# Kernel tuning notes

Measured on AMD Instinct MI355X. Metric: run time of the kernel, lower is better.

The kernel has to match this reference:

```python
import jax, jax.numpy as jnp
from jax import lax
import numpy as np

B, DIM, H, W = 1, 48, 192, 192
HEADS, K, DIL = 2, 7, 3
HD = DIM // HEADS
HID = int(DIM * 2.66)  # 127 (Restormer GEGLU hidden)
EPS = 1e-5


def _window_starts(L, Kk, D):
    # NATTEN window-start rule: keep phase i % D, shift window inside bounds.
    s = np.zeros(L, dtype=np.int32)
    for i in range(L):
        if D <= 1:
            st = max(i - Kk // 2, 0)
            if i + Kk // 2 >= L:
                st = L - Kk
        else:
            st = i - (Kk // 2) * D
            if st < 0:
                st = i % D
            elif i + (Kk // 2) * D >= L:
                imodd = i % D
                a = (L // D) * D
                b = L - a
                if imodd < b:
                    st = L - b + imodd - 2 * (Kk // 2) * D
                else:
                    st = a + imodd - Kk * D
        s[i] = st
    return s


def _nbr_tables(L, Kk, D):
    st = _window_starts(L, Kk, D)
    idx = st[:, None] + np.arange(Kk)[None, :] * D          # [L, K] absolute neighbor idx
    pb = (st - np.arange(L)) // D                            # signed offset of window start (in dilation units)
    pb = pb[:, None] + (Kk - 1) + np.arange(Kk)[None, :]     # [L, K] rpb index in [0, 2K-2]
    return jnp.asarray(idx), jnp.asarray(pb)

IH, PBH = _nbr_tables(H, K, DIL)
IW, PBW = _nbr_tables(W, K, DIL)


def layernorm(x, w, b):  # channel LN on NCHW (WithBias, biased var)
    mu = x.mean(1, keepdims=True)
    var = ((x - mu) ** 2).mean(1, keepdims=True)
    return (x - mu) / jnp.sqrt(var + EPS) * w[None, :, None, None] + b[None, :, None, None]


def na2d(x, qkv_w, qkv_b, rpb, proj_w, proj_b):
    # x: NCHW -> BHWC
    t = x.transpose(0, 2, 3, 1)
    qkv = t @ qkv_w.T + qkv_b                                # [B,H,W,3*DIM]
    qkv = qkv.reshape(B, H, W, 3, HEADS, HD)
    q, k, v = qkv[:, :, :, 0], qkv[:, :, :, 1], qkv[:, :, :, 2]
    q = q * (HD ** -0.5)
    # gather dilated 7x7 neighborhoods: [B, H, K, W, K, heads, hd]
    kn = k[:, IH[:, :, None, None], IW[None, None, :, :]]
    vn = v[:, IH[:, :, None, None], IW[None, None, :, :]]
    attn = jnp.einsum('bijnc,bixjync->bijnxy', q, kn)        # [B,H,W,heads,K,K]
    bias = rpb[:, PBH][:, :, :, PBW]                         # [heads,H,K,W,K]
    attn = attn + bias.transpose(1, 3, 0, 2, 4)
    attn = jax.nn.softmax(attn.reshape(B, H, W, HEADS, K * K), axis=-1)
    attn = attn.reshape(B, H, W, HEADS, K, K)
    out = jnp.einsum('bijnxy,bixjync->bijnc', attn, vn).reshape(B, H, W, DIM)
    out = out @ proj_w.T + proj_b
    return out.transpose(0, 3, 1, 2)


def chan_mod(x, eca_w):  # ECA-style gate: GAP -> 1D conv over channels -> sigmoid
    p = x.mean((2, 3))                                       # [B,C]
    y = lax.conv_general_dilated(p[:, None, :], eca_w[None, None, :], (1,), [(3, 3)],
                                 dimension_numbers=('NCH', 'OIH', 'NCH'))[:, 0, :]
    return jax.nn.sigmoid(y)[:, :, None, None]


def ffn(x, w_in, w_dw, w_out):  # conv-GEGLU
    t = jnp.einsum('bchw,oc->bohw', x, w_in)                 # 1x1: DIM -> 2*HID
    t = lax.conv_general_dilated(t, w_dw, (1, 1), [(1, 1), (1, 1)],
                                 feature_group_count=2 * HID,
                                 dimension_numbers=('NCHW', 'OIHW', 'NCHW'))
    x1, x2 = t[:, :HID], t[:, HID:]
    g = jax.nn.gelu(x1, approximate=False) * x2
    return jnp.einsum('bchw,oc->bohw', g, w_out)             # 1x1: HID -> DIM


def setup_inputs() -> dict:
    key = jax.random.key(0)
    ks = jax.random.split(key, 10)
    d = {
        'x': jax.random.normal(ks[0], (B, DIM, H, W), jnp.float32),
        'ln1_w': jnp.ones((DIM,), jnp.float32),
        'ln1_b': jnp.zeros((DIM,), jnp.float32),
        'qkv_w': jax.random.normal(ks[1], (3 * DIM, DIM), jnp.float32) * 0.05,
        'qkv_b': jnp.zeros((3 * DIM,), jnp.float32),
        'rpb': jax.random.normal(ks[2], (HEADS, 2 * K - 1, 2 * K - 1), jnp.float32) * 0.02,
        'proj_w': jax.random.normal(ks[3], (DIM, DIM), jnp.float32) * 0.05,
        'proj_b': jnp.zeros((DIM,), jnp.float32),
        'eca_w': jax.random.normal(ks[4], (7,), jnp.float32) * 0.1,
        'ln2_w': jnp.ones((DIM,), jnp.float32),
        'ln2_b': jnp.zeros((DIM,), jnp.float32),
        'w_in': jax.random.normal(ks[5], (2 * HID, DIM), jnp.float32) * 0.05,
        'w_dw': jax.random.normal(ks[6], (2 * HID, 1, 3, 3), jnp.float32) * 0.05,
        'w_out': jax.random.normal(ks[7], (DIM, HID), jnp.float32) * 0.05,
    }
    return d


def reference(x, ln1_w, ln1_b, qkv_w, qkv_b, rpb, proj_w, proj_b, eca_w,
              ln2_w, ln2_b, w_in, w_dw, w_out):
    xn1 = layernorm(x, ln1_w, ln1_b)
    x = x + na2d(xn1, qkv_w, qkv_b, rpb, proj_w, proj_b) * chan_mod(xn1, eca_w)
    x = x + ffn(layernorm(x, ln2_w, ln2_b), w_in, w_dw, w_out)
    return x
```

## Files before the change

kernel.cpp:

```cpp
#include <hip/hip_runtime.h>
#include <hip/hip_bf16.h>
#include <math.h>

#define HW_ (192*192)
#define Wd 192
#define HIDc 127
#define NBLK1 (HW_/64)

#define O_LN1W 0
#define O_QKVW 96
#define O_QKVB 7008
#define O_RPB  7152
#define O_PROJW 7490
#define O_PROJB 9794
#define O_ECA  9842
#define O_LN2W 9849
#define O_WIN  9945
#define O_WDW  22137
#define O_WOUT 24423
#define WTS_LEN 30519

typedef unsigned short ushort_t;
typedef _Float16 half2_t __attribute__((ext_vector_type(2)));

__device__ __forceinline__ float b2f(__hip_bfloat16 v){ return __bfloat162float(v); }
__device__ __forceinline__ float u2f(ushort_t h){ return __uint_as_float(((unsigned)h)<<16); }
__device__ __forceinline__ ushort_t f2u(float f){
    __hip_bfloat16 h = __float2bfloat16(f);
    union { __hip_bfloat16 b; ushort_t u; } c; c.b = h; return c.u;
}
__device__ __forceinline__ void up2(unsigned u, float& a, float& b){
    a = __uint_as_float(u << 16);
    b = __uint_as_float(u & 0xffff0000u);
}
__device__ __forceinline__ unsigned pkh2(float a, float b){
    half2_t h; h[0] = (_Float16)a; h[1] = (_Float16)b;
    union { half2_t h; unsigned u; } c; c.h = h; return c.u;
}
__device__ __forceinline__ half2_t u2h2(unsigned u){
    union { unsigned u; half2_t h; } c; c.u = u; return c.h;
}
__device__ __forceinline__ float dot2h(half2_t a, half2_t b, float c){
    return c + (float)a[0]*(float)b[0] + (float)a[1]*(float)b[1];
}

__device__ __forceinline__ int wstart(int i){
    if (i < 9) return i % 3;
    if (i >= 183) return 171 + (i % 3);
    return i - 9;
}

__device__ __forceinline__ float dot48bf(const uint4* wr, const float* xr){
    float acc = 0.f;
    #pragma unroll
    for (int c8 = 0; c8 < 6; c8++){
        uint4 u = wr[c8];
        float f0,f1,f2,f3,f4,f5,f6,f7;
        up2(u.x,f0,f1); up2(u.y,f2,f3); up2(u.z,f4,f5); up2(u.w,f6,f7);
        acc += f0*xr[8*c8]   + f1*xr[8*c8+1] + f2*xr[8*c8+2] + f3*xr[8*c8+3]
             + f4*xr[8*c8+4] + f5*xr[8*c8+5] + f6*xr[8*c8+6] + f7*xr[8*c8+7];
    }
    return acc;
}

__global__ void convert_kernel(
    const void* p0, const void* p1, const void* p2, const void* p3,
    const void* p4, const void* p5, const void* p6, const void* p7,
    const void* p8, const void* p9, const void* p10, const void* p11,
    const void* p12, const ushort_t* __restrict__ xu, int* __restrict__ mode_out,
    float* __restrict__ wts, ushort_t* __restrict__ qkvbf, ushort_t* __restrict__ woutTbf,
    ushort_t* __restrict__ winbf, ushort_t* __restrict__ projbf)
{
    __shared__ int sbad;
    if (threadIdx.x == 0) sbad = 0;
    __syncthreads();
    {
        unsigned u = xu[2*threadIdx.x];
        float f = __uint_as_float(u << 16);
        if (!(fabsf(f) < 100.f)) atomicAdd(&sbad, 1);
    }
    __syncthreads();
    const int md = (sbad > 16) ? 1 : 0;
    if (blockIdx.x == 0 && threadIdx.x == 0) mode_out[0] = md;

    const void* ps[13] = {p0,p1,p2,p3,p4,p5,p6,p7,p8,p9,p10,p11,p12};
    const int sz[13]  = {48,48,6912,144,338,2304,48,7,48,48,12192,2286,6096};
    const int off[13] = {O_LN1W,48,O_QKVW,O_QKVB,O_RPB,O_PROJW,O_PROJB,O_ECA,
                         O_LN2W,9897,O_WIN,O_WDW,O_WOUT};
    int b = blockIdx.x;
    if (b >= 13){
        if (b == 13){
            if (md){
                const float* s = (const float*)p2;
                for (int i = threadIdx.x; i < 6912; i += 256) qkvbf[i] = f2u(s[i]);
            } else {
                const ushort_t* s = (const ushort_t*)p2;
                for (int i = threadIdx.x; i < 6912; i += 256) qkvbf[i] = s[i];
            }
        } else if (b == 14){
            if (md){
                const float* s = (const float*)p12;
                for (int i = threadIdx.x; i < 6096; i += 256){
                    int c = i / 48, o = i - c*48;
                    woutTbf[i] = f2u(s[o*127 + c]);
                }
            } else {
                const ushort_t* s = (const ushort_t*)p12;
                for (int i = threadIdx.x; i < 6096; i += 256){
                    int c = i / 48, o = i - c*48;
                    woutTbf[i] = s[o*127 + c];
                }
            }
        } else if (b == 15){
            if (md){
                const float* s = (const float*)p10;
                for (int i = threadIdx.x; i < 12192; i += 256) winbf[i] = f2u(s[i]);
            } else {
                const ushort_t* s = (const ushort_t*)p10;
                for (int i = threadIdx.x; i < 12192; i += 256) winbf[i] = s[i];
            }
        } else {
            if (md){
                const float* s = (const float*)p5;
                for (int i = threadIdx.x; i < 2304; i += 256) projbf[i] = f2u(s[i]);
            } else {
                const ushort_t* s = (const ushort_t*)p5;
                for (int i = threadIdx.x; i < 2304; i += 256) projbf[i] = s[i];
            }
        }
        return;
    }
    int n = sz[b];
    float* dst = wts + off[b];
    if (md){
        const float* s = (const float*)ps[b];
        for (int i = threadIdx.x; i < n; i += 256) dst[i] = s[i];
    } else {
        const __hip_bfloat16* s = (const __hip_bfloat16*)ps[b];
        for (int i = threadIdx.x; i < n; i += 256) dst[i] = b2f(s[i]);
    }
}

__global__ __launch_bounds__(384) void ln1qkv_kernel(
    const void* __restrict__ x, const int* __restrict__ mode,
    const float* __restrict__ wts, const ushort_t* __restrict__ qkvbf,
    ushort_t* __restrict__ q, ushort_t* __restrict__ k, ushort_t* __restrict__ v,
    float* __restrict__ chpart)
{
    __shared__ float sx[64*49];

    const int tid  = threadIdx.x;
    const int px_l = tid & 63;
    const int r6   = __builtin_amdgcn_readfirstlane(tid >> 6);
    const int p0   = blockIdx.x * 64;
    const int p    = p0 + px_l;

    if (mode[0]){
        const float* xf = (const float*)x;
        for (int idx = tid; idx < 64*48; idx += 384){
            int c = idx >> 6, pl = idx & 63;
            sx[pl*49 + c] = xf[c*HW_ + p0 + pl];
        }
    } else {
        const __hip_bfloat16* xb = (const __hip_bfloat16*)x;
        for (int idx = tid; idx < 64*48; idx += 384){
            int c = idx >> 6, pl = idx & 63;
            sx[pl*49 + c] = b2f(xb[c*HW_ + p0 + pl]);
        }
    }
    __syncthreads();

    float xr[48];
    float mu = 0.f;
    #pragma unroll
    for (int c = 0; c < 48; c++){ xr[c] = sx[px_l*49 + c]; mu += xr[c]; }
    mu *= (1.f/48.f);
    float var = 0.f;
    #pragma unroll
    for (int c = 0; c < 48; c++){ float d = xr[c]-mu; var += d*d; }
    var *= (1.f/48.f);
    float rs = rsqrtf(var + 1e-5f);
    #pragma unroll
    for (int c = 0; c < 48; c++)
        xr[c] = (xr[c]-mu)*rs*wts[O_LN1W + c] + wts[O_LN1W + 48 + c];

    if (tid < 64){
        #pragma unroll
        for (int c = 0; c < 48; c++){
            float s = xr[c];
            s += __shfl_xor(s, 1);  s += __shfl_xor(s, 2);  s += __shfl_xor(s, 4);
            s += __shfl_xor(s, 8);  s += __shfl_xor(s, 16); s += __shfl_xor(s, 32);
            if (tid == 0) chpart[blockIdx.x*48 + c] = s;
        }
    }

    const int rbase = r6 * 24;
    const float scale = (r6 < 2) ? 0.20412414523193154f : 1.0f;
    float ov[24];
    #pragma unroll 4
    for (int ro = 0; ro < 24; ro++){
        int r = rbase + ro;
        float acc = wts[O_QKVB + r]
                  + dot48bf((const uint4*)(qkvbf + r*48), xr);
        ov[ro] = acc * scale;
    }

    unsigned int pk[12];
    #pragma unroll
    for (int d = 0; d < 12; d++)
        pk[d] = pkh2(ov[2*d], ov[2*d+1]);
    ushort_t* tp = (r6 >> 1) == 0 ? q : ((r6 >> 1) == 1 ? k : v);
    uint4* dst4 = (uint4*)(tp + (size_t)p*48 + (r6 & 1)*24);
    dst4[0] = make_uint4(pk[0], pk[1], pk[2],  pk[3]);
    dst4[1] = make_uint4(pk[4], pk[5], pk[6],  pk[7]);
    dst4[2] = make_uint4(pk[8], pk[9], pk[10], pk[11]);
}

__global__ __launch_bounds__(256) void gatefuse_kernel(
    const float* __restrict__ chpart, const float* __restrict__ wts,
    float* __restrict__ gate)
{
    __shared__ float sm[48];
    const int t = threadIdx.x;
    if (t < 192){
        const int ch = t >> 2, qq = t & 3;
        float acc = 0.f;
        #pragma unroll 4
        for (int b = qq; b < NBLK1; b += 4)
            acc += chpart[b*48 + ch];
        acc += __shfl_xor(acc, 1);
        acc += __shfl_xor(acc, 2);
        if (qq == 0) sm[ch] = acc * (1.f / (float)HW_);
    }
    __syncthreads();
    if (t < 48){
        float a = 0.f;
        for (int kk = 0; kk < 7; kk++){
            int cc = t + kk - 3;
            if (cc >= 0 && cc < 48) a += wts[O_ECA + kk] * sm[cc];
        }
        gate[t] = 1.f / (1.f + expf(-a));
    }
}

__global__ __launch_bounds__(128) void attn_kernel(
    const ushort_t* __restrict__ q, const ushort_t* __restrict__ k,
    const ushort_t* __restrict__ v, const float* __restrict__ wts,
    ushort_t* __restrict__ aout)
{
    __shared__ float srpb[169];
    const int head = blockIdx.y;
    const int tid  = threadIdx.x;
    for (int i0 = tid; i0 < 169; i0 += 128) srpb[i0] = wts[O_RPB + head*169 + i0];
    __syncthreads();

    const int p4   = tid & 3;
    const int px_l = tid >> 2;
    const int px   = blockIdx.x * 32 + px_l;
    const int i = px / Wd, j = px % Wd;
    const int sti = wstart(i), stj = wstart(j);
    const int pbi = (sti - i) / 3 + 6;
    const int pbj = (stj - j) / 3 + 6;
    const int choff = head * 24;

    half2_t qh[12];
    {
        const uint4* qp = (const uint4*)(q + (size_t)px*48 + choff);
        uint4 q0 = qp[0], q1 = qp[1], q2 = qp[2];
        qh[0]=u2h2(q0.x); qh[1]=u2h2(q0.y); qh[2] =u2h2(q0.z); qh[3] =u2h2(q0.w);
        qh[4]=u2h2(q1.x); qh[5]=u2h2(q1.y); qh[6] =u2h2(q1.z); qh[7] =u2h2(q1.w);
        qh[8]=u2h2(q2.x); qh[9]=u2h2(q2.y); qh[10]=u2h2(q2.z); qh[11]=u2h2(q2.w);
    }

    float s = 0.f;
    float acc[24];
    #pragma unroll
    for (int c = 0; c < 24; c++) acc[c] = 0.f;

    #pragma unroll 4
    for (int tt = 0; tt < 13; tt++){
        int n = 4*tt + p4;
        const bool bad = (n > 48);
        if (bad) n = 48;
        int xx = (n * 147) >> 10;
        int yy = n - 7*xx;
        int ii = sti + 3*xx, jj = stj + 3*yy;
        const size_t nb = (size_t)(ii*Wd + jj)*48 + choff;
        const uint4* kp = (const uint4*)(k + nb);
        const uint4* vp = (const uint4*)(v + nb);
        uint4 K0 = kp[0], K1 = kp[1], K2 = kp[2];
        uint4 V0 = vp[0], V1 = vp[1], V2 = vp[2];
        float d = 0.f;
        d = dot2h(u2h2(K0.x), qh[0],  d);
        d = dot2h(u2h2(K0.y), qh[1],  d);
        d = dot2h(u2h2(K0.z), qh[2],  d);
        d = dot2h(u2h2(K0.w), qh[3],  d);
        d = dot2h(u2h2(K1.x), qh[4],  d);
        d = dot2h(u2h2(K1.y), qh[5],  d);
        d = dot2h(u2h2(K1.z), qh[6],  d);
        d = dot2h(u2h2(K1.w), qh[7],  d);
        d = dot2h(u2h2(K2.x), qh[8],  d);
        d = dot2h(u2h2(K2.y), qh[9],  d);
        d = dot2h(u2h2(K2.z), qh[10], d);
        d = dot2h(u2h2(K2.w), qh[11], d);
        float sc = d + srpb[(pbi+xx)*13 + (pbj+yy)];
        sc = fminf(sc, 80.f);
        if (bad) sc = -1e30f;
        float p = __expf(sc);
        s += p;
        half2_t vv;
        vv=u2h2(V0.x); acc[0] +=p*(float)vv[0]; acc[1] +=p*(float)vv[1];
        vv=u2h2(V0.y); acc[2] +=p*(float)vv[0]; acc[3] +=p*(float)vv[1];
        vv=u2h2(V0.z); acc[4] +=p*(float)vv[0]; acc[5] +=p*(float)vv[1];
        vv=u2h2(V0.w); acc[6] +=p*(float)vv[0]; acc[7] +=p*(float)vv[1];
        vv=u2h2(V1.x); acc[8] +=p*(float)vv[0]; acc[9] +=p*(float)vv[1];
        vv=u2h2(V1.y); acc[10]+=p*(float)vv[0]; acc[11]+=p*(float)vv[1];
        vv=u2h2(V1.z); acc[12]+=p*(float)vv[0]; acc[13]+=p*(float)vv[1];
        vv=u2h2(V1.w); acc[14]+=p*(float)vv[0]; acc[15]+=p*(float)vv[1];
        vv=u2h2(V2.x); acc[16]+=p*(float)vv[0]; acc[17]+=p*(float)vv[1];
        vv=u2h2(V2.y); acc[18]+=p*(float)vv[0]; acc[19]+=p*(float)vv[1];
        vv=u2h2(V2.z); acc[20]+=p*(float)vv[0]; acc[21]+=p*(float)vv[1];
        vv=u2h2(V2.w); acc[22]+=p*(float)vv[0]; acc[23]+=p*(float)vv[1];
    }

    s += __shfl_xor(s, 1);
    s += __shfl_xor(s, 2);
    #pragma unroll
    for (int c = 0; c < 24; c++){
        acc[c] += __shfl_xor(acc[c], 1);
        acc[c] += __shfl_xor(acc[c], 2);
    }
    const float inv = 1.f / s;
    if (p4 == 0){
        #pragma unroll
        for (int c = 0; c < 6; c++)
            aout[(size_t)(choff + c)*HW_ + px] = f2u(acc[c] * inv);
    } else if (p4 == 1){
        #pragma unroll
        for (int c = 0; c < 6; c++)
            aout[(size_t)(choff + 6 + c)*HW_ + px] = f2u(acc[6 + c] * inv);
    } else if (p4 == 2){
        #pragma unroll
        for (int c = 0; c < 6; c++)
            aout[(size_t)(choff + 12 + c)*HW_ + px] = f2u(acc[12 + c] * inv);
    } else {
        #pragma unroll
        for (int c = 0; c < 6; c++)
            aout[(size_t)(choff + 18 + c)*HW_ + px] = f2u(acc[18 + c] * inv);
    }
}

__global__ __launch_bounds__(256) void projpw1_kernel(
    const ushort_t* __restrict__ aout, const float* __restrict__ wts,
    const ushort_t* __restrict__ projbf, const float* __restrict__ gate,
    const void* __restrict__ x, const int* __restrict__ mode,
    float* __restrict__ x2, const ushort_t* __restrict__ winbf,
    ushort_t* __restrict__ tout)
{
    __shared__ float sa[64*49];

    const int tid  = threadIdx.x;
    const int px_l = tid & 63;
    const int og   = __builtin_amdgcn_readfirstlane(tid >> 6);
    const int px   = blockIdx.x * 64 + px_l;

    float ar[48];
    #pragma unroll
    for (int c = 0; c < 48; c++) ar[c] = u2f(aout[(size_t)c*HW_ + px]);

    const float* xf = (const float*)x;
    const __hip_bfloat16* xb = (const __hip_bfloat16*)x;
    const int md = mode[0];
    const int ob = og * 12;
    #pragma unroll 2
    for (int oo = 0; oo < 12; oo++){
        int o = ob + oo;
        float accp = wts[O_PROJB + o]
                   + dot48bf((const uint4*)(projbf + o*48), ar);
        float res = md ? xf[o*HW_ + px] : b2f(xb[o*HW_ + px]);
        float xv = res + accp * gate[o];
        x2[o*HW_ + px] = xv;
        sa[px_l*49 + o] = xv;
    }
    __syncthreads();

    float xr[48];
    float mu = 0.f;
    #pragma unroll
    for (int c = 0; c < 48; c++){ xr[c] = sa[px_l*49 + c]; mu += xr[c]; }
    mu *= (1.f/48.f);
    float var = 0.f;
    #pragma unroll
    for (int c = 0; c < 48; c++){ float dd = xr[c]-mu; var += dd*dd; }
    var *= (1.f/48.f);
    float rs = rsqrtf(var + 1e-5f);
    #pragma unroll
    for (int c = 0; c < 48; c++)
        xr[c] = (xr[c]-mu)*rs*wts[O_LN2W + c] + wts[O_LN2W + 48 + c];

    const int base = og * 64;
    for (int t2 = 0; t2 < 64; t2 += 2){
        int o0 = base + t2;
        if (o0 >= 254) break;
        const uint4* wA = (const uint4*)(winbf + o0*48);
        const uint4* wB = (const uint4*)(winbf + min(o0+1,253)*48);
        float accA = 0.f, accB = 0.f;
        #pragma unroll
        for (int c8 = 0; c8 < 6; c8++){
            uint4 ua = wA[c8];
            uint4 ub = wB[c8];
            float a0,a1,a2,a3,a4,a5,a6,a7, b0,b1,b2,b3,b4,b5,b6,b7;
            up2(ua.x,a0,a1); up2(ua.y,a2,a3); up2(ua.z,a4,a5); up2(ua.w,a6,a7);
            up2(ub.x,b0,b1); up2(ub.y,b2,b3); up2(ub.z,b4,b5); up2(ub.w,b6,b7);
            accA += a0*xr[8*c8]   + a1*xr[8*c8+1] + a2*xr[8*c8+2] + a3*xr[8*c8+3]
                  + a4*xr[8*c8+4] + a5*xr[8*c8+5] + a6*xr[8*c8+6] + a7*xr[8*c8+7];
            accB += b0*xr[8*c8]   + b1*xr[8*c8+1] + b2*xr[8*c8+2] + b3*xr[8*c8+3]
                  + b4*xr[8*c8+4] + b5*xr[8*c8+5] + b6*xr[8*c8+6] + b7*xr[8*c8+7];
        }
        tout[(size_t)o0*HW_ + px] = f2u(accA);
        if (o0+1 < 254) tout[(size_t)(o0+1)*HW_ + px] = f2u(accB);
    }
}

__global__ __launch_bounds__(256) void dw_kernel(
    const ushort_t* __restrict__ t, const float* __restrict__ wts,
    ushort_t* __restrict__ g)
{
    const int ch = blockIdx.y;
    const int pp = (blockIdx.x * 256 + threadIdx.x) * 4;
    const int i  = pp / Wd, j = pp % Wd;
    float w1[9], w2[9];
    #pragma unroll
    for (int s2 = 0; s2 < 9; s2++){
        w1[s2] = wts[O_WDW + ch*9 + s2];
        w2[s2] = wts[O_WDW + (ch+HIDc)*9 + s2];
    }
    const ushort_t* t1 = t + (size_t)ch * HW_;
    const ushort_t* t2 = t + (size_t)(ch+HIDc) * HW_;
    float a10=0.f,a11=0.f,a12=0.f,a13=0.f;
    float a20=0.f,a21=0.f,a22=0.f,a23=0.f;
    #pragma unroll
    for (int di = 0; di < 3; di++){
        int ii = i + di - 1;
        if (ii < 0 || ii >= 192) continue;
        int base = ii*Wd + j;
        float wa = w1[di*3], wb = w1[di*3+1], wc = w1[di*3+2];
        {
            uint2 mm = *(const uint2*)(t1 + base);
            float c0,c1,c2,c3; up2(mm.x,c0,c1); up2(mm.y,c2,c3);
            float cm = (j > 0)     ? u2f(t1[base-1]) : 0.f;
            float cp = (j+4 < Wd)  ? u2f(t1[base+4]) : 0.f;
            a10 += wa*cm + wb*c0 + wc*c1;
            a11 += wa*c0 + wb*c1 + wc*c2;
            a12 += wa*c1 + wb*c2 + wc*c3;
            a13 += wa*c2 + wb*c3 + wc*cp;
        }
        wa = w2[di*3]; wb = w2[di*3+1]; wc = w2[di*3+2];
        {
            uint2 mm = *(const uint2*)(t2 + base);
            float c0,c1,c2,c3; up2(mm.x,c0,c1); up2(mm.y,c2,c3);
            float cm = (j > 0)     ? u2f(t2[base-1]) : 0.f;
            float cp = (j+4 < Wd)  ? u2f(t2[base+4]) : 0.f;
            a20 += wa*cm + wb*c0 + wc*c1;
            a21 += wa*c0 + wb*c1 + wc*c2;
            a22 += wa*c1 + wb*c2 + wc*c3;
            a23 += wa*c2 + wb*c3 + wc*cp;
        }
    }
    const float RS2 = 0.70710678118654752f;
    float g0 = a10 * 0.5f * (1.f + erff(a10 * RS2)) * a20;
    float g1 = a11 * 0.5f * (1.f + erff(a11 * RS2)) * a21;
    float g2 = a12 * 0.5f * (1.f + erff(a12 * RS2)) * a22;
    float g3 = a13 * 0.5f * (1.f + erff(a13 * RS2)) * a23;
    uint2 pk;
    pk.x = (unsigned)f2u(g0) | ((unsigned)f2u(g1) << 16);
    pk.y = (unsigned)f2u(g2) | ((unsigned)f2u(g3) << 16);
    *(uint2*)(g + (size_t)ch*HW_ + pp) = pk;
}

__global__ __launch_bounds__(128) void pw2_kernel(
    const ushort_t* __restrict__ g, const ushort_t* __restrict__ woutTbf,
    const float* __restrict__ x2, void* __restrict__ outv,
    const int* __restrict__ mode)
{
    const int ob = blockIdx.y * 12;
    const int p  = blockIdx.x * 128 + threadIdx.x;
    float acc[12];
    #pragma unroll
    for (int o = 0; o < 12; o++) acc[o] = 0.f;
    #pragma unroll 4
    for (int c = 0; c < 127; c++){
        float gv = u2f(g[(size_t)c*HW_ + p]);
        const unsigned* wr = (const unsigned*)(woutTbf + c*48 + ob);
        #pragma unroll
        for (int d = 0; d < 6; d++){
            float w0, w1;
            up2(wr[d], w0, w1);
            acc[2*d]   += w0*gv;
            acc[2*d+1] += w1*gv;
        }
    }
    if (mode[0]){
        float* out = (float*)outv;
        #pragma unroll
        for (int o = 0; o < 12; o++){
            int oc = ob + o;
            out[(size_t)oc*HW_ + p] = x2[(size_t)oc*HW_ + p] + acc[o];
        }
    } else {
        __hip_bfloat16* out = (__hip_bfloat16*)outv;
        #pragma unroll
        for (int o = 0; o < 12; o++){
            int oc = ob + o;
            out[(size_t)oc*HW_ + p] =
                __float2bfloat16(x2[(size_t)oc*HW_ + p] + acc[o]);
        }
    }
}

extern "C" void kernel_launch(void* const* d_in, const int* in_sizes, int n_in,
                              void* d_out, int out_size, void* d_ws, size_t ws_size,
                              hipStream_t stream)
{
    (void)in_sizes; (void)n_in; (void)out_size;

    char* ws = (char*)d_ws;
    ushort_t* q    = (ushort_t*)(ws);
    ushort_t* k    = (ushort_t*)(ws + 3538944);
    ushort_t* v    = (ushort_t*)(ws + 7077888);
    float*    x2   = (float*)   (ws + 10616832);
    ushort_t* t    = (ushort_t*)(ws + 17694720);
    ushort_t* g    = (ushort_t*)(ws);
    float*    gate = (float*)   (ws + 36421632);
    int*      mode = (int*)     (ws + 36421824);
    float*    wts  = (float*)   (ws + 36421840);
    float*    chpart=(float*)   (ws + 36543920);
    ushort_t* qkvbf   = (ushort_t*)(ws + 36654512);
    ushort_t* woutTbf = (ushort_t*)(ws + 36668336);
    ushort_t* winbf   = (ushort_t*)(ws + 36680528);
    ushort_t* projbf  = (ushort_t*)(ws + 36704912);
    ushort_t* aout    = (ushort_t*)(ws + 36709520);

    size_t need = 36709520 + 3538944;
    if (ws_size < need) return;

    convert_kernel<<<17, 256, 0, stream>>>(
        d_in[1], d_in[2], d_in[3], d_in[4], d_in[5], d_in[6], d_in[7],
        d_in[8], d_in[9], d_in[10], d_in[11], d_in[12], d_in[13],
        (const ushort_t*)d_in[0], mode, wts, qkvbf, woutTbf, winbf, projbf);

    ln1qkv_kernel<<<dim3(NBLK1), 384, 0, stream>>>(d_in[0], mode, wts, qkvbf,
                                                   q, k, v, chpart);
    gatefuse_kernel<<<1, 256, 0, stream>>>(chpart, wts, gate);
    attn_kernel<<<dim3(HW_/32, 2), 128, 0, stream>>>(q, k, v, wts, aout);
    projpw1_kernel<<<dim3(HW_/64), 256, 0, stream>>>(aout, wts, projbf, gate,
                                                     d_in[0], mode, x2, winbf, t);
    dw_kernel<<<dim3(HW_/1024, 127), 256, 0, stream>>>(t, wts, g);
    pw2_kernel<<<dim3(HW_/128, 4), 128, 0, stream>>>(g, woutTbf, x2, d_out, mode);
}
```

Before: 246.2 us.

## Use fp16 packed dot products in projpw1 and double its block size

The attention output, projection weights and pw1 weights are now stored as fp16 instead of bf16. projpw1 keeps its activations packed as half2, so the dot products work on packed pairs and need no bf16 unpacking. The block grows from 256 to 512 threads, so each wave group handles 6 projection outputs and 32 pw1 outputs instead of 12 and 64, and fewer registers are live per thread. The risk is fp16 range and precision loss on activations, and the dot2h helper may still lower to scalar conversions rather than a packed dot instruction.

```diff
diff --git a/kernel.cpp b/kernel.cpp
--- a/kernel.cpp
+++ b/kernel.cpp
@@ -29,6 +29,10 @@
     __hip_bfloat16 h = __float2bfloat16(f);
     union { __hip_bfloat16 b; ushort_t u; } c; c.b = h; return c.u;
 }
+__device__ __forceinline__ ushort_t f2h(float f){
+    _Float16 h = (_Float16)f;
+    union { _Float16 h; ushort_t u; } c; c.h = h; return c.u;
+}
 __device__ __forceinline__ void up2(unsigned u, float& a, float& b){
     a = __uint_as_float(u << 16);
     b = __uint_as_float(u & 0xffff0000u);
@@ -42,6 +46,18 @@
 }
 __device__ __forceinline__ float dot2h(half2_t a, half2_t b, float c){
     return c + (float)a[0]*(float)b[0] + (float)a[1]*(float)b[1];
+}
+__device__ __forceinline__ float dot48h(const uint4* wr, const unsigned* xu){
+    float acc = 0.f;
+    #pragma unroll
+    for (int c8 = 0; c8 < 6; c8++){
+        uint4 u = wr[c8];
+        acc = dot2h(u2h2(u.x), u2h2(xu[4*c8+0]), acc);
+        acc = dot2h(u2h2(u.y), u2h2(xu[4*c8+1]), acc);
+        acc = dot2h(u2h2(u.z), u2h2(xu[4*c8+2]), acc);
+        acc = dot2h(u2h2(u.w), u2h2(xu[4*c8+3]), acc);
+    }
+    return acc;
 }
 
 __device__ __forceinline__ int wstart(int i){
@@ -114,18 +130,18 @@
         } else if (b == 15){
             if (md){
                 const float* s = (const float*)p10;
-                for (int i = threadIdx.x; i < 12192; i += 256) winbf[i] = f2u(s[i]);
+                for (int i = threadIdx.x; i < 12192; i += 256) winbf[i] = f2h(s[i]);
             } else {
                 const ushort_t* s = (const ushort_t*)p10;
-                for (int i = threadIdx.x; i < 12192; i += 256) winbf[i] = s[i];
+                for (int i = threadIdx.x; i < 12192; i += 256) winbf[i] = f2h(u2f(s[i]));
             }
         } else {
             if (md){
                 const float* s = (const float*)p5;
-                for (int i = threadIdx.x; i < 2304; i += 256) projbf[i] = f2u(s[i]);
+                for (int i = threadIdx.x; i < 2304; i += 256) projbf[i] = f2h(s[i]);
             } else {
                 const ushort_t* s = (const ushort_t*)p5;
-                for (int i = threadIdx.x; i < 2304; i += 256) projbf[i] = s[i];
+                for (int i = threadIdx.x; i < 2304; i += 256) projbf[i] = f2h(u2f(s[i]));
             }
         }
         return;
@@ -334,23 +350,23 @@
     if (p4 == 0){
         #pragma unroll
         for (int c = 0; c < 6; c++)
-            aout[(size_t)(choff + c)*HW_ + px] = f2u(acc[c] * inv);
+            aout[(size_t)(choff + c)*HW_ + px] = f2h(acc[c] * inv);
     } else if (p4 == 1){
         #pragma unroll
         for (int c = 0; c < 6; c++)
-            aout[(size_t)(choff + 6 + c)*HW_ + px] = f2u(acc[6 + c] * inv);
+            aout[(size_t)(choff + 6 + c)*HW_ + px] = f2h(acc[6 + c] * inv);
     } else if (p4 == 2){
         #pragma unroll
         for (int c = 0; c < 6; c++)
-            aout[(size_t)(choff + 12 + c)*HW_ + px] = f2u(acc[12 + c] * inv);
+            aout[(size_t)(choff + 12 + c)*HW_ + px] = f2h(acc[12 + c] * inv);
     } else {
         #pragma unroll
         for (int c = 0; c < 6; c++)
-            aout[(size_t)(choff + 18 + c)*HW_ + px] = f2u(acc[18 + c] * inv);
-    }
-}
-
-__global__ __launch_bounds__(256) void projpw1_kernel(
+            aout[(size_t)(choff + 18 + c)*HW_ + px] = f2h(acc[18 + c] * inv);
+    }
+}
+
+__global__ __launch_bounds__(512) void projpw1_kernel(
     const ushort_t* __restrict__ aout, const float* __restrict__ wts,
     const ushort_t* __restrict__ projbf, const float* __restrict__ gate,
     const void* __restrict__ x, const int* __restrict__ mode,
@@ -364,19 +380,23 @@
     const int og   = __builtin_amdgcn_readfirstlane(tid >> 6);
     const int px   = blockIdx.x * 64 + px_l;
 
-    float ar[48];
-    #pragma unroll
-    for (int c = 0; c < 48; c++) ar[c] = u2f(aout[(size_t)c*HW_ + px]);
+    unsigned au[24];
+    #pragma unroll
+    for (int c = 0; c < 24; c++){
+        unsigned lo = aout[(size_t)(2*c    )*HW_ + px];
+        unsigned hi = aout[(size_t)(2*c + 1)*HW_ + px];
+        au[c] = lo | (hi << 16);
+    }
 
     const float* xf = (const float*)x;
     const __hip_bfloat16* xb = (const __hip_bfloat16*)x;
     const int md = mode[0];
-    const int ob = og * 12;
-    #pragma unroll 2
-    for (int oo = 0; oo < 12; oo++){
+    const int ob = og * 6;
+    #pragma unroll
+    for (int oo = 0; oo < 6; oo++){
         int o = ob + oo;
         float accp = wts[O_PROJB + o]
-                   + dot48bf((const uint4*)(projbf + o*48), ar);
+                   + dot48h((const uint4*)(projbf + o*48), au);
         float res = md ? xf[o*HW_ + px] : b2f(xb[o*HW_ + px]);
         float xv = res + accp * gate[o];
         x2[o*HW_ + px] = xv;
@@ -398,25 +418,16 @@
     for (int c = 0; c < 48; c++)
         xr[c] = (xr[c]-mu)*rs*wts[O_LN2W + c] + wts[O_LN2W + 48 + c];
 
-    const int base = og * 64;
-    for (int t2 = 0; t2 < 64; t2 += 2){
+    unsigned xu2[24];
+    #pragma unroll
+    for (int c = 0; c < 24; c++) xu2[c] = pkh2(xr[2*c], xr[2*c+1]);
+
+    const int base = og * 32;
+    for (int t2 = 0; t2 < 32; t2 += 2){
         int o0 = base + t2;
         if (o0 >= 254) break;
-        const uint4* wA = (const uint4*)(winbf + o0*48);
-        const uint4* wB = (const uint4*)(winbf + min(o0+1,253)*48);
-        float accA = 0.f, accB = 0.f;
-        #pragma unroll
-        for (int c8 = 0; c8 < 6; c8++){
-            uint4 ua = wA[c8];
-            uint4 ub = wB[c8];
-            float a0,a1,a2,a3,a4,a5,a6,a7, b0,b1,b2,b3,b4,b5,b6,b7;
-            up2(ua.x,a0,a1); up2(ua.y,a2,a3); up2(ua.z,a4,a5); up2(ua.w,a6,a7);
-            up2(ub.x,b0,b1); up2(ub.y,b2,b3); up2(ub.z,b4,b5); up2(ub.w,b6,b7);
-            accA += a0*xr[8*c8]   + a1*xr[8*c8+1] + a2*xr[8*c8+2] + a3*xr[8*c8+3]
-                  + a4*xr[8*c8+4] + a5*xr[8*c8+5] + a6*xr[8*c8+6] + a7*xr[8*c8+7];
-            accB += b0*xr[8*c8]   + b1*xr[8*c8+1] + b2*xr[8*c8+2] + b3*xr[8*c8+3]
-                  + b4*xr[8*c8+4] + b5*xr[8*c8+5] + b6*xr[8*c8+6] + b7*xr[8*c8+7];
-        }
+        float accA = dot48h((const uint4*)(winbf + o0*48), xu2);
+        float accB = dot48h((const uint4*)(winbf + min(o0+1,253)*48), xu2);
         tout[(size_t)o0*HW_ + px] = f2u(accA);
         if (o0+1 < 254) tout[(size_t)(o0+1)*HW_ + px] = f2u(accB);
     }
@@ -553,7 +564,7 @@
                                                    q, k, v, chpart);
     gatefuse_kernel<<<1, 256, 0, stream>>>(chpart, wts, gate);
     attn_kernel<<<dim3(HW_/32, 2), 128, 0, stream>>>(q, k, v, wts, aout);
-    projpw1_kernel<<<dim3(HW_/64), 256, 0, stream>>>(aout, wts, projbf, gate,
+    projpw1_kernel<<<dim3(HW_/64), 512, 0, stream>>>(aout, wts, projbf, gate,
                                                      d_in[0], mode, x2, winbf, t);
     dw_kernel<<<dim3(HW_/1024, 127), 256, 0, stream>>>(t, wts, g);
     pw2_kernel<<<dim3(HW_/128, 4), 128, 0, stream>>>(g, woutTbf, x2, d_out, mode);
```

Measured after the change: 245.9 us. About the same (-0.1%).
